# Kernel optimization log

Measured on AMD Instinct MI355X. Metric: run time of the kernel, lower is better.

## Reference

```python
import jax, jax.numpy as jnp
import numpy as np

H = 64  # hidden_dim

def _lstm_dir(x, Wih, Whh, bih, bhh, reverse):
    # x: [B, T, D]; Wih: [4H, D]; Whh: [4H, H]; PyTorch gate order i,f,g,o
    B, T, _ = x.shape
    if reverse:
        x = x[:, ::-1, :]
    # Precompute input contribution to all gates: [B, T, 4H]
    xg = jnp.einsum('btd,gd->btg', x, Wih) + (bih + bhh)
    h0 = jnp.zeros((B, H), x.dtype)
    c0 = jnp.zeros((B, H), x.dtype)

    def step(carry, xg_t):
        h, c = carry
        g = xg_t + h @ Whh.T  # [B, 4H]
        i, f, gg, o = jnp.split(g, 4, axis=-1)
        i = jax.nn.sigmoid(i)
        f = jax.nn.sigmoid(f)
        gg = jnp.tanh(gg)
        o = jax.nn.sigmoid(o)
        c = f * c + i * gg
        h = o * jnp.tanh(c)
        return (h, c), h

    (hT, cT), hs = jax.lax.scan(step, (h0, c0), jnp.swapaxes(xg, 0, 1))
    hs = jnp.swapaxes(hs, 0, 1)  # [B, T, H]
    if reverse:
        hs = hs[:, ::-1, :]
    return hs, hT

def _forward(x, Wih_l0_f, Whh_l0_f, bih_l0_f, bhh_l0_f,
             Wih_l0_b, Whh_l0_b, bih_l0_b, bhh_l0_b,
             Wih_l1_f, Whh_l1_f, bih_l1_f, bhh_l1_f,
             Wih_l1_b, Whh_l1_b, bih_l1_b, bhh_l1_b,
             fc1_W, fc1_b, fc2_W, fc2_b):
    xt = jnp.transpose(x, (0, 2, 1))  # [B, 512, 3]
    # Layer 0 (bidirectional)
    hs_f, _ = _lstm_dir(xt, Wih_l0_f, Whh_l0_f, bih_l0_f, bhh_l0_f, False)
    hs_b, _ = _lstm_dir(xt, Wih_l0_b, Whh_l0_b, bih_l0_b, bhh_l0_b, True)
    y0 = jnp.concatenate([hs_f, hs_b], axis=-1)  # [B, 512, 2H]
    # (inter-layer dropout is identity in eval mode)
    # Layer 1 (bidirectional); only final hidden states needed
    _, hT_f = _lstm_dir(y0, Wih_l1_f, Whh_l1_f, bih_l1_f, bhh_l1_f, False)
    _, hT_b = _lstm_dir(y0, Wih_l1_b, Whh_l1_b, bih_l1_b, bhh_l1_b, True)
    h = jnp.concatenate([hT_f, hT_b], axis=-1)  # [B, 2H]
    h = jax.nn.relu(h @ fc1_W.T + fc1_b)
    return h @ fc2_W.T + fc2_b  # [B, num_classes]

def setup_inputs() -> dict:
    key = jax.random.key(0)
    ks = iter(jax.random.split(key, 32))
    B, T, C = 1024, 512, 3
    d = {}
    d['x'] = jax.random.normal(next(ks), (B, C, T), dtype=jnp.float32)
    # PyTorch-style bias init: forget-gate bias = 1, rest 0
    bias = jnp.zeros((4 * H,), jnp.float32).at[H:2 * H].set(1.0)
    for layer, din in [(0, C), (1, 2 * H)]:
        for dirn in ['f', 'b']:
            d[f'Wih_l{layer}_{dirn}'] = jax.random.normal(next(ks), (4 * H, din), dtype=jnp.float32) * 0.1
            d[f'Whh_l{layer}_{dirn}'] = jax.random.normal(next(ks), (4 * H, H), dtype=jnp.float32) * 0.1
            d[f'bih_l{layer}_{dirn}'] = bias
            d[f'bhh_l{layer}_{dirn}'] = jnp.zeros((4 * H,), jnp.float32)
    d['fc1_W'] = jax.random.normal(next(ks), (H, 2 * H), dtype=jnp.float32) * 0.1
    d['fc1_b'] = jnp.zeros((H,), jnp.float32)
    d['fc2_W'] = jax.random.normal(next(ks), (2, H), dtype=jnp.float32) * 0.1
    d['fc2_b'] = jnp.zeros((2,), jnp.float32)
    return d

def reference(x, Wih_l0_f, Whh_l0_f, bih_l0_f, bhh_l0_f,
              Wih_l0_b, Whh_l0_b, bih_l0_b, bhh_l0_b,
              Wih_l1_f, Whh_l1_f, bih_l1_f, bhh_l1_f,
              Wih_l1_b, Whh_l1_b, bih_l1_b, bhh_l1_b,
              fc1_W, fc1_b, fc2_W, fc2_b):
    return _forward(x, Wih_l0_f, Whh_l0_f, bih_l0_f, bhh_l0_f,
                    Wih_l0_b, Whh_l0_b, bih_l0_b, bhh_l0_b,
                    Wih_l1_f, Whh_l1_f, bih_l1_f, bhh_l1_f,
                    Wih_l1_b, Whh_l1_b, bih_l1_b, bhh_l1_b,
                    fc1_W, fc1_b, fc2_W, fc2_b)
```

## Files before the change

### kernel.cpp

```cpp
#include <hip/hip_runtime.h>
#include <stdint.h>

typedef __attribute__((ext_vector_type(8))) short short8;
typedef __attribute__((ext_vector_type(4))) float f32x4;

#define TT 512
#define LSTR 136
#define XS 516

static __device__ __forceinline__ uint32_t f2bf_u(float f){
  union { float f; uint32_t u; } v; v.f = f;
  return (v.u + 0x7fffu + ((v.u >> 16) & 1u)) >> 16;
}
static __device__ __forceinline__ short8 w8f32(const float* p){
  float4 a = *(const float4*)p;
  float4 b = *(const float4*)(p + 4);
  short8 r;
  r[0] = (short)f2bf_u(a.x); r[1] = (short)f2bf_u(a.y);
  r[2] = (short)f2bf_u(a.z); r[3] = (short)f2bf_u(a.w);
  r[4] = (short)f2bf_u(b.x); r[5] = (short)f2bf_u(b.y);
  r[6] = (short)f2bf_u(b.z); r[7] = (short)f2bf_u(b.w);
  return r;
}
static __device__ __forceinline__ float sigx(float x){
  float e = __builtin_amdgcn_exp2f(-1.442695040888963f * x);
  return __builtin_amdgcn_rcpf(1.f + e);
}
static __device__ __forceinline__ float tanhx(float x){
  float e = __builtin_amdgcn_exp2f(-2.885390081777927f * x);
  return fmaf(__builtin_amdgcn_rcpf(1.f + e), 2.f, -1.f);
}
static __device__ __forceinline__ void lds_barrier(){
  asm volatile("s_waitcnt lgkmcnt(0)" ::: "memory");
  __builtin_amdgcn_s_barrier();
}
#define MF(A,B,C) __builtin_amdgcn_mfma_f32_16x16x32_bf16((A),(B),(C),0,0,0)
#define SWZ(x) __int_as_float(__builtin_amdgcn_ds_swizzle(__float_as_int(x), 0x201F))

__global__ __launch_bounds__(256, 2) void lstm_l0(
    const float* __restrict__ x,
    const float* __restrict__ Wih_f, const float* __restrict__ Whh_f,
    const float* __restrict__ bih_f, const float* __restrict__ bhh_f,
    const float* __restrict__ Wih_b, const float* __restrict__ Whh_b,
    const float* __restrict__ bih_b, const float* __restrict__ bhh_b,
    unsigned short* __restrict__ y0)
{
  const int tid = threadIdx.x;
  const int wv = tid >> 6, lane = tid & 63;
  const int quad = lane >> 4, m16 = lane & 15;
  const int dir = blockIdx.y;
  const int bbase = blockIdx.x * 4;
  const float* Wih = dir ? Wih_b : Wih_f;
  const float* Whh = dir ? Whh_b : Whh_f;
  const float* bih = dir ? bih_b : bih_f;
  const float* bhh = dir ? bhh_b : bhh_f;

  __shared__ __align__(16) unsigned short sZ[2][4][LSTR];
  __shared__ __align__(16) float sX[12 * XS];

  const int copy = m16 >> 2;
  const int batch = m16 & 3;
  const int unit = 16 * wv + 4 * copy + quad;
  const bool selA = (copy & 1) != 0;
  const bool selB = (copy & 2) != 0;

  short8 aH[4][2];
  const int gm = (m16 & 3) * 64 + (m16 >> 2);
  #pragma unroll
  for (int k = 0; k < 4; k++){
    const int g = gm + 4 * (4 * wv + k);
    aH[k][0] = w8f32(Whh + g * 64 + quad * 8);
    aH[k][1] = w8f32(Whh + g * 64 + 32 + quad * 8);
  }
  float Wf[4][3];
  f32x4 biasF;
  #pragma unroll
  for (int r = 0; r < 4; r++){
    biasF[r] = bih[r * 64 + unit] + bhh[r * 64 + unit];
    #pragma unroll
    for (int d = 0; d < 3; d++) Wf[r][d] = Wih[(r * 64 + unit) * 3 + d];
  }

  for (int idx = tid; idx < 2 * 4 * LSTR; idx += 256)
    ((unsigned short*)sZ)[idx] = 0;
  for (int i4 = tid; i4 < 1536; i4 += 256){
    const int row = i4 >> 7, t4 = (i4 & 127) * 4;
    *(float4*)&sX[row * XS + t4] = *(const float4*)(x + (size_t)bbase * 1536 + row * 512 + t4);
  }
  __syncthreads();

  const int xrow = 3 * batch;
  float c = 0.f, h = 0.f;
  const f32x4 z4 = {0.f, 0.f, 0.f, 0.f};

#define FFCOMP(F, TIDX) do { \
    float x0_ = sX[xrow * XS + (TIDX)]; \
    float x1_ = sX[(xrow + 1) * XS + (TIDX)]; \
    float x2_ = sX[(xrow + 2) * XS + (TIDX)]; \
    _Pragma("unroll") \
    for (int r_ = 0; r_ < 4; r_++) \
      F[r_] = fmaf(Wf[r_][2], x2_, fmaf(Wf[r_][1], x1_, fmaf(Wf[r_][0], x0_, biasF[r_]))); \
  } while(0)

  f32x4 FBa, FBb;
  {
    const int t0_ = dir ? (TT - 1) : 0;
    FFCOMP(FBa, t0_);
  }

#define L0STEP(S, P, FC, FN) do { \
    const int p1_ = (P) ^ 1; \
    short8 bh0 = *(const short8*)&sZ[P][batch][     quad * 8]; \
    short8 bh1 = *(const short8*)&sZ[P][batch][32 + quad * 8]; \
    if (wv == 3 && lane < 32 && (S) > 0){ \
      const int tprev = dir ? (TT - (S)) : ((S) - 1); \
      const int br_ = lane >> 3, cc_ = lane & 7; \
      uint4 v_ = *(const uint4*)&sZ[P][br_][cc_ * 8]; \
      *(uint4*)(y0 + ((size_t)(bbase + br_) * TT + tprev) * 128 + dir * 64 + cc_ * 8) = v_; \
    } \
    f32x4 C0 = MF(aH[0][0], bh0, z4); \
    f32x4 C1 = MF(aH[1][0], bh0, z4); \
    f32x4 C2 = MF(aH[2][0], bh0, z4); \
    f32x4 C3 = MF(aH[3][0], bh0, z4); \
    C0 = MF(aH[0][1], bh1, C0); \
    C1 = MF(aH[1][1], bh1, C1); \
    C2 = MF(aH[2][1], bh1, C2); \
    C3 = MF(aH[3][1], bh1, C3); \
    { int sn_ = (S) + 1; if (sn_ > TT - 1) sn_ = TT - 1; \
      const int tn_ = dir ? (TT - 1 - sn_) : sn_; \
      FFCOMP(FN, tn_); \
    } \
    __builtin_amdgcn_sched_barrier(0); \
    { \
      float g0_ = (selB ? (selA ? C3[0] : C2[0]) : (selA ? C1[0] : C0[0])) + FC[0]; \
      float g1_ = (selB ? (selA ? C3[1] : C2[1]) : (selA ? C1[1] : C0[1])) + FC[1]; \
      float g2_ = (selB ? (selA ? C3[2] : C2[2]) : (selA ? C1[2] : C0[2])) + FC[2]; \
      float g3_ = (selB ? (selA ? C3[3] : C2[3]) : (selA ? C1[3] : C0[3])) + FC[3]; \
      float ii_ = sigx(g0_), ff_ = sigx(g1_), gg_ = tanhx(g2_), oo_ = sigx(g3_); \
      c = fmaf(ff_, c, ii_ * gg_); \
      h = oo_ * tanhx(c); \
      sZ[p1_][batch][unit] = (unsigned short)f2bf_u(h); \
    } \
    __builtin_amdgcn_sched_barrier(0); \
    lds_barrier(); \
  } while(0)

  for (int s = 0; s < TT; s += 2){
    L0STEP(s,     0, FBa, FBb);
    L0STEP(s + 1, 1, FBb, FBa);
  }
#undef L0STEP
#undef FFCOMP

  if (wv == 3 && lane < 32){
    const int tl = dir ? 0 : (TT - 1);
    const int br = lane >> 3, cc = lane & 7;
    uint4 v = *(const uint4*)&sZ[0][br][cc * 8];
    *(uint4*)(y0 + ((size_t)(bbase + br) * TT + tl) * 128 + dir * 64 + cc * 8) = v;
  }
}

__global__ __launch_bounds__(512, 2) void lstm_l1(
    const unsigned short* __restrict__ y0,
    const float* __restrict__ Wih_f, const float* __restrict__ Whh_f,
    const float* __restrict__ bih_f, const float* __restrict__ bhh_f,
    const float* __restrict__ Wih_b, const float* __restrict__ Whh_b,
    const float* __restrict__ bih_b, const float* __restrict__ bhh_b,
    float* __restrict__ hT)
{
  const int tid = threadIdx.x;
  const int wv = tid >> 6, lane = tid & 63;
  const int quad = lane >> 4, m16 = lane & 15;
  const int dir = blockIdx.y;
  const int bbase = blockIdx.x * 8;
  const float* Wih = dir ? Wih_b : Wih_f;
  const float* Whh = dir ? Whh_b : Whh_f;
  const float* bih = dir ? bih_b : bih_f;
  const float* bhh = dir ? bhh_b : bhh_f;

  __shared__ __align__(16) unsigned short sZ[2][8][LSTR];
  __shared__ __align__(16) unsigned short sY[4][8][LSTR];

  short8 aY[2][4], aH[2][2];
  f32x4 biasv[2];
  const int gm = (m16 & 3) * 64 + (m16 >> 2);
  #pragma unroll
  for (int i = 0; i < 2; i++){
    const int rt = 2 * wv + i;
    const int g = gm + 4 * rt;
    #pragma unroll
    for (int kt = 0; kt < 4; kt++) aY[i][kt] = w8f32(Wih + g * 128 + kt * 32 + quad * 8);
    aH[i][0] = w8f32(Whh + g * 64 + quad * 8);
    aH[i][1] = w8f32(Whh + g * 64 + 32 + quad * 8);
    const int gu = 4 * rt + quad;
    #pragma unroll
    for (int r = 0; r < 4; r++) biasv[i][r] = bih[r * 64 + gu] + bhh[r * 64 + gu];
  }

  for (int idx = tid; idx < 2 * 8 * LSTR; idx += 512)
    ((unsigned short*)sZ)[idx] = 0;

  const bool stager = (lane < 16);
  const size_t sgbase = (size_t)(bbase + wv) * TT * 128 + (size_t)lane * 8;
  float4 hA = make_float4(0.f,0.f,0.f,0.f), hB = make_float4(0.f,0.f,0.f,0.f);
  if (stager){
    #pragma unroll
    for (int k = 0; k < 4; k++){
      const int tk = dir ? (TT - 1 - k) : k;
      *(float4*)&sY[k][wv][lane * 8] = *(const float4*)(y0 + sgbase + (size_t)tk * 128);
    }
    const int t4 = dir ? (TT - 5) : 4, t5 = dir ? (TT - 6) : 5;
    hA = *(const float4*)(y0 + sgbase + (size_t)t4 * 128);
    hB = *(const float4*)(y0 + sgbase + (size_t)t5 * 128);
  }
  __syncthreads();

  const int m8 = m16 & 7;
  const bool sel0 = (m16 < 8);
  const int colw = 8 * wv + quad + ((m16 >> 3) << 2);
  float c = 0.f, h = 0.f;
  const f32x4 z4 = {0.f, 0.f, 0.f, 0.f};

  const int SLOTU = 8 * LSTR;
  const unsigned short* yb = &sY[0][0][0] + (sel0 ? 0 : SLOTU) + m8 * LSTR + quad * 8;

#define FFMM(SL, FB0, FB1) do { \
    short8 by0 = *(const short8*)(yb + (SL) * SLOTU); \
    short8 by1 = *(const short8*)(yb + (SL) * SLOTU + 32); \
    short8 by2 = *(const short8*)(yb + (SL) * SLOTU + 64); \
    short8 by3 = *(const short8*)(yb + (SL) * SLOTU + 96); \
    FB0 = MF(aY[0][0], by0, biasv[0]); \
    FB1 = MF(aY[1][0], by0, biasv[1]); \
    FB0 = MF(aY[0][1], by1, FB0);  FB1 = MF(aY[1][1], by1, FB1); \
    FB0 = MF(aY[0][2], by2, FB0);  FB1 = MF(aY[1][2], by2, FB1); \
    FB0 = MF(aY[0][3], by3, FB0);  FB1 = MF(aY[1][3], by3, FB1); \
  } while(0)

#define FFSWZ(FB0, FB1, G0, G1) do { \
    float w10_ = SWZ(FB1[0]), w11_ = SWZ(FB1[1]), w12_ = SWZ(FB1[2]), w13_ = SWZ(FB1[3]); \
    float w00_ = SWZ(FB0[0]), w01_ = SWZ(FB0[1]), w02_ = SWZ(FB0[2]), w03_ = SWZ(FB0[3]); \
    G0[0] = sel0 ? FB0[0] : w10_;  G0[1] = sel0 ? FB0[1] : w11_; \
    G0[2] = sel0 ? FB0[2] : w12_;  G0[3] = sel0 ? FB0[3] : w13_; \
    G1[0] = sel0 ? w00_ : FB1[0];  G1[1] = sel0 ? w01_ : FB1[1]; \
    G1[2] = sel0 ? w02_ : FB1[2];  G1[3] = sel0 ? w03_ : FB1[3]; \
  } while(0)

  f32x4 Ga0, Ga1, Gb0, Gb1, FBT0, FBT1;
  FFMM(0, FBT0, FBT1);
  FFSWZ(FBT0, FBT1, Ga0, Ga1);
  lds_barrier();

#define NONLIN1(R0, R1, GC, P1) do { \
    float g0_ = (sel0 ? (R0)[0] : (R1)[0]) + GC[0]; \
    float g1_ = (sel0 ? (R0)[1] : (R1)[1]) + GC[1]; \
    float g2_ = (sel0 ? (R0)[2] : (R1)[2]) + GC[2]; \
    float g3_ = (sel0 ? (R0)[3] : (R1)[3]) + GC[3]; \
    float ii_ = sigx(g0_), ff_ = sigx(g1_), gg_ = tanhx(g2_), oo_ = sigx(g3_); \
    c = fmaf(ff_, c, ii_ * gg_); \
    h = oo_ * tanhx(c); \
    sZ[P1][m8][colw] = (unsigned short)f2bf_u(h); \
  } while(0)

#define STAGE(S, WRSL, HOLD) do { \
    if (stager){ \
      *(float4*)&sY[WRSL][wv][lane * 8] = HOLD; \
      int sg_ = (S) + 6; if (sg_ > TT - 1) sg_ = TT - 1; \
      const int tg_ = dir ? (TT - 1 - sg_) : sg_; \
      HOLD = *(const float4*)(y0 + sgbase + (size_t)tg_ * 128); \
    } \
  } while(0)

#define L1STEPA(S, SLFF, WRSL, HOLD, GC) do { \
    short8 bh0 = *(const short8*)&sZ[0][m8][     quad * 8]; \
    short8 bh1 = *(const short8*)&sZ[0][m8][32 + quad * 8]; \
    f32x4 R0 = MF(aH[0][0], bh0, z4); \
    f32x4 R1 = MF(aH[1][0], bh0, z4); \
    R0 = MF(aH[0][1], bh1, R0); \
    R1 = MF(aH[1][1], bh1, R1); \
    FFMM(SLFF, FBT0, FBT1); \
    STAGE(S, WRSL, HOLD); \
    __builtin_amdgcn_sched_barrier(0); \
    NONLIN1(R0, R1, GC, 1); \
    __builtin_amdgcn_sched_barrier(0); \
    lds_barrier(); \
  } while(0)

#define L1STEPB(S, WRSL, HOLD, GC, GN0, GN1) do { \
    short8 bh0 = *(const short8*)&sZ[1][m8][     quad * 8]; \
    short8 bh1 = *(const short8*)&sZ[1][m8][32 + quad * 8]; \
    f32x4 R0 = MF(aH[0][0], bh0, z4); \
    f32x4 R1 = MF(aH[1][0], bh0, z4); \
    R0 = MF(aH[0][1], bh1, R0); \
    R1 = MF(aH[1][1], bh1, R1); \
    FFSWZ(FBT0, FBT1, GN0, GN1); \
    STAGE(S, WRSL, HOLD); \
    __builtin_amdgcn_sched_barrier(0); \
    NONLIN1(R0, R1, GC, 0); \
    if ((S) == TT - 1){ \
      hT[(size_t)(bbase + m8) * 128 + dir * 64 + colw] = h; \
    } \
    __builtin_amdgcn_sched_barrier(0); \
    lds_barrier(); \
  } while(0)

  for (int s = 0; s < TT; s += 4){
    L1STEPA(s,     2, 0, hA, Ga0);
    L1STEPB(s + 1,    1, hB, Ga1, Gb0, Gb1);
    L1STEPA(s + 2, 0, 2, hA, Gb0);
    L1STEPB(s + 3,    3, hB, Gb1, Ga0, Ga1);
  }
#undef L1STEPA
#undef L1STEPB
#undef STAGE
#undef NONLIN1
#undef FFSWZ
#undef FFMM
}

__global__ __launch_bounds__(256, 1) void fc_kernel(
    const float* __restrict__ hT,
    const float* __restrict__ w1, const float* __restrict__ b1,
    const float* __restrict__ w2, const float* __restrict__ b2,
    float* __restrict__ out)
{
  __shared__ float sh[4][64];
  const int wave = threadIdx.x >> 6, lane = threadIdx.x & 63;
  const int b = blockIdx.x * 4 + wave;
  float acc = b1[lane];
  const float* hrow = hT + (size_t)b * 128;
  #pragma unroll
  for (int k = 0; k < 128; k += 4){
    float4 h4 = *(const float4*)(hrow + k);
    float4 w4 = *(const float4*)(w1 + lane * 128 + k);
    acc = fmaf(w4.x, h4.x, acc);
    acc = fmaf(w4.y, h4.y, acc);
    acc = fmaf(w4.z, h4.z, acc);
    acc = fmaf(w4.w, h4.w, acc);
  }
  sh[wave][lane] = fmaxf(acc, 0.f);
  __syncthreads();
  if (lane < 2){
    float a = b2[lane];
    #pragma unroll
    for (int k = 0; k < 64; k++) a = fmaf(w2[lane * 64 + k], sh[wave][k], a);
    out[(size_t)b * 2 + lane] = a;
  }
}

extern "C" void kernel_launch(void* const* d_in, const int* in_sizes, int n_in,
                              void* d_out, int out_size, void* d_ws, size_t ws_size,
                              hipStream_t stream){
  (void)in_sizes; (void)n_in; (void)out_size; (void)ws_size;
  const float* x     = (const float*)d_in[0];
  const float* Wih0f = (const float*)d_in[1];
  const float* Whh0f = (const float*)d_in[2];
  const float* bih0f = (const float*)d_in[3];
  const float* bhh0f = (const float*)d_in[4];
  const float* Wih0b = (const float*)d_in[5];
  const float* Whh0b = (const float*)d_in[6];
  const float* bih0b = (const float*)d_in[7];
  const float* bhh0b = (const float*)d_in[8];
  const float* Wih1f = (const float*)d_in[9];
  const float* Whh1f = (const float*)d_in[10];
  const float* bih1f = (const float*)d_in[11];
  const float* bhh1f = (const float*)d_in[12];
  const float* Wih1b = (const float*)d_in[13];
  const float* Whh1b = (const float*)d_in[14];
  const float* bih1b = (const float*)d_in[15];
  const float* bhh1b = (const float*)d_in[16];
  const float* fc1W  = (const float*)d_in[17];
  const float* fc1b  = (const float*)d_in[18];
  const float* fc2W  = (const float*)d_in[19];
  const float* fc2b  = (const float*)d_in[20];
  float* out = (float*)d_out;

  unsigned short* y0 = (unsigned short*)d_ws;
  float* hT = (float*)((char*)d_ws + (size_t)1024 * TT * 128 * 2);

  lstm_l0<<<dim3(256, 2), dim3(256), 0, stream>>>(x, Wih0f, Whh0f, bih0f, bhh0f,
                                                  Wih0b, Whh0b, bih0b, bhh0b, y0);
  lstm_l1<<<dim3(128, 2), dim3(512), 0, stream>>>(y0, Wih1f, Whh1f, bih1f, bhh1f,
                                                  Wih1b, Whh1b, bih1b, bhh1b, hT);
  fc_kernel<<<dim3(256), dim3(256), 0, stream>>>(hT, fc1W, fc1b, fc2W, fc2b, out);
}
```

Measured before the change: 513.3 us.

## Split layer-1 LSTM gate tiles across 16 waves instead of 8

The layer-1 recurrent kernel now launches 1024 threads per block, so each wave owns one 16-row gate tile instead of two. This halves per-wave MFMA and nonlinearity work on the serial recurrence critical path. The gate bias plus input projection is fed straight into the recurrent MFMA accumulator, and only half the lanes write h. In exchange, the per-step block barrier must synchronize twice as many waves, half the lanes do redundant nonlinearity work, and fewer blocks may fit per CU.

```diff
diff --git a/kernel.cpp b/kernel.cpp
--- a/kernel.cpp
+++ b/kernel.cpp
@@ -160,7 +160,7 @@
   }
 }
 
-__global__ __launch_bounds__(512, 2) void lstm_l1(
+__global__ __launch_bounds__(1024, 4) void lstm_l1(
     const unsigned short* __restrict__ y0,
     const float* __restrict__ Wih_f, const float* __restrict__ Whh_f,
     const float* __restrict__ bih_f, const float* __restrict__ bhh_f,
@@ -181,27 +181,23 @@
   __shared__ __align__(16) unsigned short sZ[2][8][LSTR];
   __shared__ __align__(16) unsigned short sY[4][8][LSTR];
 
-  short8 aY[2][4], aH[2][2];
-  f32x4 biasv[2];
+  short8 aY[4], aH[2];
+  f32x4 biasv;
   const int gm = (m16 & 3) * 64 + (m16 >> 2);
-  #pragma unroll
-  for (int i = 0; i < 2; i++){
-    const int rt = 2 * wv + i;
-    const int g = gm + 4 * rt;
-    #pragma unroll
-    for (int kt = 0; kt < 4; kt++) aY[i][kt] = w8f32(Wih + g * 128 + kt * 32 + quad * 8);
-    aH[i][0] = w8f32(Whh + g * 64 + quad * 8);
-    aH[i][1] = w8f32(Whh + g * 64 + 32 + quad * 8);
-    const int gu = 4 * rt + quad;
-    #pragma unroll
-    for (int r = 0; r < 4; r++) biasv[i][r] = bih[r * 64 + gu] + bhh[r * 64 + gu];
-  }
-
-  for (int idx = tid; idx < 2 * 8 * LSTR; idx += 512)
+  const int g = gm + 4 * wv;
+  #pragma unroll
+  for (int kt = 0; kt < 4; kt++) aY[kt] = w8f32(Wih + g * 128 + kt * 32 + quad * 8);
+  aH[0] = w8f32(Whh + g * 64 + quad * 8);
+  aH[1] = w8f32(Whh + g * 64 + 32 + quad * 8);
+  const int unit = 4 * wv + quad;
+  #pragma unroll
+  for (int r = 0; r < 4; r++) biasv[r] = bih[r * 64 + unit] + bhh[r * 64 + unit];
+
+  for (int idx = tid; idx < 2 * 8 * LSTR; idx += 1024)
     ((unsigned short*)sZ)[idx] = 0;
 
-  const bool stager = (lane < 16);
-  const size_t sgbase = (size_t)(bbase + wv) * TT * 128 + (size_t)lane * 8;
+  const bool stager = (wv < 8) && (lane < 16);
+  const size_t sgbase = (size_t)(bbase + (wv & 7)) * TT * 128 + (size_t)(lane & 15) * 8;
   float4 hA = make_float4(0.f,0.f,0.f,0.f), hB = make_float4(0.f,0.f,0.f,0.f);
   if (stager){
     #pragma unroll
@@ -217,48 +213,40 @@
 
   const int m8 = m16 & 7;
   const bool sel0 = (m16 < 8);
-  const int colw = 8 * wv + quad + ((m16 >> 3) << 2);
   float c = 0.f, h = 0.f;
-  const f32x4 z4 = {0.f, 0.f, 0.f, 0.f};
 
   const int SLOTU = 8 * LSTR;
   const unsigned short* yb = &sY[0][0][0] + (sel0 ? 0 : SLOTU) + m8 * LSTR + quad * 8;
 
-#define FFMM(SL, FB0, FB1) do { \
+#define FFMM(SL, FB) do { \
     short8 by0 = *(const short8*)(yb + (SL) * SLOTU); \
     short8 by1 = *(const short8*)(yb + (SL) * SLOTU + 32); \
     short8 by2 = *(const short8*)(yb + (SL) * SLOTU + 64); \
     short8 by3 = *(const short8*)(yb + (SL) * SLOTU + 96); \
-    FB0 = MF(aY[0][0], by0, biasv[0]); \
-    FB1 = MF(aY[1][0], by0, biasv[1]); \
-    FB0 = MF(aY[0][1], by1, FB0);  FB1 = MF(aY[1][1], by1, FB1); \
-    FB0 = MF(aY[0][2], by2, FB0);  FB1 = MF(aY[1][2], by2, FB1); \
-    FB0 = MF(aY[0][3], by3, FB0);  FB1 = MF(aY[1][3], by3, FB1); \
-  } while(0)
-
-#define FFSWZ(FB0, FB1, G0, G1) do { \
-    float w10_ = SWZ(FB1[0]), w11_ = SWZ(FB1[1]), w12_ = SWZ(FB1[2]), w13_ = SWZ(FB1[3]); \
-    float w00_ = SWZ(FB0[0]), w01_ = SWZ(FB0[1]), w02_ = SWZ(FB0[2]), w03_ = SWZ(FB0[3]); \
-    G0[0] = sel0 ? FB0[0] : w10_;  G0[1] = sel0 ? FB0[1] : w11_; \
-    G0[2] = sel0 ? FB0[2] : w12_;  G0[3] = sel0 ? FB0[3] : w13_; \
-    G1[0] = sel0 ? w00_ : FB1[0];  G1[1] = sel0 ? w01_ : FB1[1]; \
-    G1[2] = sel0 ? w02_ : FB1[2];  G1[3] = sel0 ? w03_ : FB1[3]; \
-  } while(0)
-
-  f32x4 Ga0, Ga1, Gb0, Gb1, FBT0, FBT1;
-  FFMM(0, FBT0, FBT1);
-  FFSWZ(FBT0, FBT1, Ga0, Ga1);
+    FB = MF(aY[0], by0, biasv); \
+    FB = MF(aY[1], by1, FB); \
+    FB = MF(aY[2], by2, FB); \
+    FB = MF(aY[3], by3, FB); \
+  } while(0)
+
+#define FFSWZ(FB, G0, G1) do { \
+    float w0_ = SWZ(FB[0]), w1_ = SWZ(FB[1]), w2_ = SWZ(FB[2]), w3_ = SWZ(FB[3]); \
+    G0[0] = sel0 ? FB[0] : w0_;  G0[1] = sel0 ? FB[1] : w1_; \
+    G0[2] = sel0 ? FB[2] : w2_;  G0[3] = sel0 ? FB[3] : w3_; \
+    G1[0] = sel0 ? w0_ : FB[0];  G1[1] = sel0 ? w1_ : FB[1]; \
+    G1[2] = sel0 ? w2_ : FB[2];  G1[3] = sel0 ? w3_ : FB[3]; \
+  } while(0)
+
+  f32x4 Ga0, Ga1, Gb0, Gb1, FBT;
+  FFMM(0, FBT);
+  FFSWZ(FBT, Ga0, Ga1);
   lds_barrier();
 
-#define NONLIN1(R0, R1, GC, P1) do { \
-    float g0_ = (sel0 ? (R0)[0] : (R1)[0]) + GC[0]; \
-    float g1_ = (sel0 ? (R0)[1] : (R1)[1]) + GC[1]; \
-    float g2_ = (sel0 ? (R0)[2] : (R1)[2]) + GC[2]; \
-    float g3_ = (sel0 ? (R0)[3] : (R1)[3]) + GC[3]; \
-    float ii_ = sigx(g0_), ff_ = sigx(g1_), gg_ = tanhx(g2_), oo_ = sigx(g3_); \
+#define NONLIN1(R, P1) do { \
+    float ii_ = sigx((R)[0]), ff_ = sigx((R)[1]), gg_ = tanhx((R)[2]), oo_ = sigx((R)[3]); \
     c = fmaf(ff_, c, ii_ * gg_); \
     h = oo_ * tanhx(c); \
-    sZ[P1][m8][colw] = (unsigned short)f2bf_u(h); \
+    if (sel0) sZ[P1][m8][unit] = (unsigned short)f2bf_u(h); \
   } while(0)
 
 #define STAGE(S, WRSL, HOLD) do { \
@@ -273,14 +261,12 @@
 #define L1STEPA(S, SLFF, WRSL, HOLD, GC) do { \
     short8 bh0 = *(const short8*)&sZ[0][m8][     quad * 8]; \
     short8 bh1 = *(const short8*)&sZ[0][m8][32 + quad * 8]; \
-    f32x4 R0 = MF(aH[0][0], bh0, z4); \
-    f32x4 R1 = MF(aH[1][0], bh0, z4); \
-    R0 = MF(aH[0][1], bh1, R0); \
-    R1 = MF(aH[1][1], bh1, R1); \
-    FFMM(SLFF, FBT0, FBT1); \
+    f32x4 R = MF(aH[0], bh0, GC); \
+    R = MF(aH[1], bh1, R); \
+    FFMM(SLFF, FBT); \
     STAGE(S, WRSL, HOLD); \
     __builtin_amdgcn_sched_barrier(0); \
-    NONLIN1(R0, R1, GC, 1); \
+    NONLIN1(R, 1); \
     __builtin_amdgcn_sched_barrier(0); \
     lds_barrier(); \
   } while(0)
@@ -288,16 +274,14 @@
 #define L1STEPB(S, WRSL, HOLD, GC, GN0, GN1) do { \
     short8 bh0 = *(const short8*)&sZ[1][m8][     quad * 8]; \
     short8 bh1 = *(const short8*)&sZ[1][m8][32 + quad * 8]; \
-    f32x4 R0 = MF(aH[0][0], bh0, z4); \
-    f32x4 R1 = MF(aH[1][0], bh0, z4); \
-    R0 = MF(aH[0][1], bh1, R0); \
-    R1 = MF(aH[1][1], bh1, R1); \
-    FFSWZ(FBT0, FBT1, GN0, GN1); \
+    f32x4 R = MF(aH[0], bh0, GC); \
+    R = MF(aH[1], bh1, R); \
+    FFSWZ(FBT, GN0, GN1); \
     STAGE(S, WRSL, HOLD); \
     __builtin_amdgcn_sched_barrier(0); \
-    NONLIN1(R0, R1, GC, 0); \
-    if ((S) == TT - 1){ \
-      hT[(size_t)(bbase + m8) * 128 + dir * 64 + colw] = h; \
+    NONLIN1(R, 0); \
+    if ((S) == TT - 1 && sel0){ \
+      hT[(size_t)(bbase + m8) * 128 + dir * 64 + unit] = h; \
     } \
     __builtin_amdgcn_sched_barrier(0); \
     lds_barrier(); \
@@ -379,7 +363,7 @@
 
   lstm_l0<<<dim3(256, 2), dim3(256), 0, stream>>>(x, Wih0f, Whh0f, bih0f, bhh0f,
                                                   Wih0b, Whh0b, bih0b, bhh0b, y0);
-  lstm_l1<<<dim3(128, 2), dim3(512), 0, stream>>>(y0, Wih1f, Whh1f, bih1f, bhh1f,
-                                                  Wih1b, Whh1b, bih1b, bhh1b, hT);
+  lstm_l1<<<dim3(128, 2), dim3(1024), 0, stream>>>(y0, Wih1f, Whh1f, bih1f, bhh1f,
+                                                   Wih1b, Whh1b, bih1b, bhh1b, hT);
   fc_kernel<<<dim3(256), dim3(256), 0, stream>>>(hT, fc1W, fc1b, fc2W, fc2b, out);
 }
```

Measured after the change: 589.6 us. 14.9% more time.
